# Optimization experiments

Hardware: AMD Instinct MI355X
Metric: run time of the kernel (lower is better)

Reference implementation:

```python
import jax, jax.numpy as jnp
import numpy as np

B, C, H, W = 4, 256, 160, 160
N = 512
REID = 128
NUM_LAYERS = 2
BINS = 7          # adaptive_avg_pool2d target (7,7)
EPS_BN = 1e-5
EPS_NORM = 1e-12  # torch F.normalize eps


def setup_inputs() -> dict:
    key = jax.random.key(0)
    ks = jax.random.split(key, 8)
    x = jax.random.normal(ks[0], (B, C, H, W), jnp.float32)
    # valid normalized boxes: x1,y1 in [0,0.7], w,h in [0.1,0.3]
    xy1 = jax.random.uniform(ks[1], (B, N, 2), minval=0.0, maxval=0.7)
    wh = jax.random.uniform(ks[2], (B, N, 2), minval=0.1, maxval=0.3)
    bboxes = jnp.concatenate([xy1, jnp.minimum(xy1 + wh, 1.0)], axis=-1)
    # conv stack params (kaiming-ish init), BN in eval mode with running stats
    conv_w = jax.random.normal(ks[3], (NUM_LAYERS, C, C, 3, 3), jnp.float32) * np.sqrt(2.0 / (C * 9)).astype(np.float32)
    conv_b = jnp.zeros((NUM_LAYERS, C), jnp.float32)
    bn_gamma = jnp.ones((NUM_LAYERS, C), jnp.float32)
    bn_beta = jnp.zeros((NUM_LAYERS, C), jnp.float32)
    bn_mean = jnp.zeros((NUM_LAYERS, C), jnp.float32)
    bn_var = jnp.ones((NUM_LAYERS, C), jnp.float32)
    # reid_embedding MLP: Linear(C, C//2) -> ReLU -> Dropout(eval) -> Linear(C//2, REID)
    w1 = jax.random.normal(ks[4], (C // 2, C), jnp.float32) * 0.01
    b1 = jnp.zeros((C // 2,), jnp.float32)
    w2 = jax.random.normal(ks[5], (REID, C // 2), jnp.float32) * 0.01
    b2 = jnp.zeros((REID,), jnp.float32)
    return dict(x=x, bboxes=bboxes, conv_w=conv_w, conv_b=conv_b,
                bn_gamma=bn_gamma, bn_beta=bn_beta, bn_mean=bn_mean, bn_var=bn_var,
                w1=w1, b1=b1, w2=w2, b2=b2)


def _conv_bn_relu(x, w, b, gamma, beta, mean, var):
    y = jax.lax.conv_general_dilated(
        x, w, window_strides=(1, 1), padding=((1, 1), (1, 1)),
        dimension_numbers=('NCHW', 'OIHW', 'NCHW')) + b[None, :, None, None]
    scale = (gamma / jnp.sqrt(var + EPS_BN))[None, :, None, None]
    y = (y - mean[None, :, None, None]) * scale + beta[None, :, None, None]
    return jax.nn.relu(y)


def _roi_pool(S, box):
    # S: (C, H+1, W+1) integral image of the feature map; box: (4,) = x1,y1,x2,y2 in [0,1]
    x1 = jnp.clip(jnp.floor(box[0] * W).astype(jnp.int32), 0, W)
    y1 = jnp.clip(jnp.floor(box[1] * H).astype(jnp.int32), 0, H)
    x2 = jnp.clip(jnp.floor(box[2] * W).astype(jnp.int32), 0, W)
    y2 = jnp.clip(jnp.floor(box[3] * H).astype(jnp.int32), 0, H)
    valid = (x2 > x1) & (y2 > y1)
    hl = jnp.maximum(y2 - y1, 1)
    wl = jnp.maximum(x2 - x1, 1)
    i = jnp.arange(BINS)
    # PyTorch adaptive_avg_pool2d binning: [floor(i*L/B), ceil((i+1)*L/B))
    hs = y1 + (i * hl) // BINS
    he = y1 + ((i + 1) * hl + BINS - 1) // BINS
    ws = x1 + (i * wl) // BINS
    we = x1 + ((i + 1) * wl + BINS - 1) // BINS
    # bin sums via integral image -> (C, 7, 7)
    s = (S[:, he[:, None], we[None, :]] - S[:, hs[:, None], we[None, :]]
         - S[:, he[:, None], ws[None, :]] + S[:, hs[:, None], ws[None, :]])
    area = ((he - hs)[:, None] * (we - ws)[None, :]).astype(S.dtype)
    # adaptive 7x7 avg pool, then global avg pool over the 7x7 grid
    pooled = jnp.mean(s / area, axis=(1, 2))  # (C,)
    return pooled, valid


def reference(x, bboxes, conv_w, conv_b, bn_gamma, bn_beta, bn_mean, bn_var, w1, b1, w2, b2):
    f = x
    for l in range(NUM_LAYERS):
        f = _conv_bn_relu(f, conv_w[l], conv_b[l], bn_gamma[l], bn_beta[l], bn_mean[l], bn_var[l])
    # integral image, zero-padded: S[b,c,y,x] = sum of f[b,c,:y,:x] -> (B, C, H+1, W+1)
    S = jnp.pad(jnp.cumsum(jnp.cumsum(f, axis=2), axis=3), ((0, 0), (0, 0), (1, 0), (1, 0)))
    pooled, valid = jax.vmap(jax.vmap(_roi_pool, in_axes=(None, 0)), in_axes=(0, 0))(S, bboxes)
    # reid_embedding MLP (dropout is identity in eval)
    h = jax.nn.relu(jnp.einsum('bnc,hc->bnh', pooled, w1) + b1)
    feat = jnp.einsum('bnh,rh->bnr', h, w2) + b2
    feat = jnp.where(valid[..., None], feat, jnp.zeros((), feat.dtype))
    norm = jnp.maximum(jnp.linalg.norm(feat, axis=-1, keepdims=True), EPS_NORM)
    return feat / norm
```

## Files before the change

### kernel.cpp

```cpp
#include <hip/hip_runtime.h>
#include <hip/hip_bf16.h>

typedef __attribute__((ext_vector_type(8))) short s16x8;
typedef __attribute__((ext_vector_type(4))) float f32x4;


__device__ __forceinline__ void async_ld16(const void* g, void* l) {
  __builtin_amdgcn_global_load_lds(
      (const __attribute__((address_space(1))) void*)g,
      (__attribute__((address_space(3))) void*)l, 16, 0, 0);
}

__global__ __launch_bounds__(256) void prep_all(
    const float* __restrict__ x,
    __hip_bfloat16* __restrict__ xpad, __hip_bfloat16* __restrict__ f1,
    const float* __restrict__ cw, __hip_bfloat16* __restrict__ wpk,
    const float* __restrict__ cb, const float* __restrict__ g,
    const float* __restrict__ bt, const float* __restrict__ mn,
    const float* __restrict__ vr, float* __restrict__ ab,
    const float* __restrict__ w1, const float* __restrict__ w2,
    float* __restrict__ w1t, float* __restrict__ w2t) {
  __shared__ float tile[32][33];
  int bi = blockIdx.x;
  if (bi < 12800) {
    int blk = bi;
    int xt = blk % 5;
    int ct = (blk / 5) & 7;
    int by = blk / 40;
    int b = by / 80, yp = by - (by / 80) * 80;
    int tx = threadIdx.x & 31, ty = threadIdx.x >> 5;
#pragma unroll
    for (int ry = 0; ry < 2; ++ry) {
      int y = yp * 2 + ry;
      const float* src = x + (((size_t)(b * 256 + ct * 32)) * 160 + y) * 160 + xt * 32 + tx;
#pragma unroll
      for (int k = 0; k < 4; k++) tile[ty * 4 + k][tx] = src[(size_t)(ty * 4 + k) * 25600];
      __syncthreads();
      __hip_bfloat16* dst =
          xpad + (((size_t)(b * 162 + y + 1)) * 162 + (xt * 32 + 1)) * 256 + ct * 32 + tx;
#pragma unroll
      for (int k = 0; k < 4; k++) {
        int xx = ty * 4 + k;
        dst[(size_t)xx * 256] = __float2bfloat16(tile[tx][xx]);
      }
      __syncthreads();
    }
  } else if (bi < 17952) {
    int e0 = bi - 12800;
    int buf = e0 / 2576; int rem = e0 - buf * 2576;
    int b = rem / 644;   int e = rem - b * 644;
    int y, xx;
    if (e < 162)      { y = 0;           xx = e; }
    else if (e < 324) { y = 161;         xx = e - 162; }
    else if (e < 484) { y = e - 324 + 1; xx = 0; }
    else              { y = e - 484 + 1; xx = 161; }
    __hip_bfloat16* p = (buf ? f1 : xpad) + (((size_t)b * 162 + y) * 162 + xx) * 256 + threadIdx.x;
    *p = __float2bfloat16(0.f);
  } else if (bi < 22560) {
    int t = (bi - 17952) * 256 + threadIdx.x;
    int ci = t & 255, co = (t >> 8) & 255, rest = t >> 16;
    int tap = rest % 9, lyr = rest / 9;
    int dy = tap / 3, dx = tap - dy * 3;
    float v = cw[((((size_t)lyr * 256 + co) * 256 + ci) * 3 + dy) * 3 + dx];
    wpk[(((size_t)lyr * 9 + tap) * 256 + co) * 256 + ci] = __float2bfloat16(v);
  } else if (bi < 22562) {
    int t = (bi - 22560) * 256 + threadIdx.x;
    float a = g[t] / sqrtf(vr[t] + 1e-5f);
    ab[t] = a;
    ab[512 + t] = (cb[t] - mn[t]) * a + bt[t];
  } else {
    int t = (bi - 22562) * 256 + threadIdx.x;
    if (t < 32768) {
      int h = t >> 8, k = t & 255;
      w1t[k * 128 + h] = w1[h * 256 + k];
    } else {
      int u = t - 32768;
      int r = u >> 7, k = u & 127;
      w2t[k * 128 + r] = w2[r * 128 + k];
    }
  }
}

__global__ __launch_bounds__(256, 2) void conv_bn_relu(
    const __hip_bfloat16* __restrict__ inp, __hip_bfloat16* __restrict__ outp,
    const __hip_bfloat16* __restrict__ wpk,
    const float* __restrict__ alpha, const float* __restrict__ beff) {
  __shared__ __align__(16) short As[128 * 64];
  __shared__ __align__(16) short Bs[256 * 64];
  const int t = threadIdx.x;
  const int mtile = ((blockIdx.x & 7) * 100) + (blockIdx.x >> 3);
  const int l = t & 63;
  const int wv = t >> 6;
  const int lr = l & 15, lq = l >> 4;
  const int wm = wv >> 1, wn = wv & 1;

  const int srow = t >> 3;
  const int koff = (((t & 7) ^ (srow & 7)) << 3);
  const short* inS = (const short*)inp;
  const short* wS = (const short*)wpk;
  long abase[4];
#pragma unroll
  for (int i = 0; i < 4; i++) {
    int p = mtile * 128 + i * 32 + srow;
    int b = p / 25600; int r = p - b * 25600; int y = r / 160; int x = r - y * 160;
    abase[i] = (((long)b * 162 + y) * 162 + x) * 256 + koff;
  }
  const long bbase = ((long)srow) * 256 + koff;

  f32x4 acc[4][8];
#pragma unroll
  for (int i = 0; i < 4; i++)
#pragma unroll
    for (int j = 0; j < 8; j++) acc[i][j] = (f32x4){0.f, 0.f, 0.f, 0.f};

#pragma unroll 1
  for (int u = 0; u < 36; ++u) {
    const int tap = u >> 2, kc = u & 3;
    const int dy = tap / 3, dx = tap - dy * 3;
    const long aoff = ((long)(dy * 162 + dx)) * 256 + kc * 64;
    const long boff = (long)tap * 65536 + kc * 64;
    __syncthreads();
#pragma unroll
    for (int i = 0; i < 4; i++)
      async_ld16(inS + abase[i] + aoff, As + i * 2048 + t * 8);
#pragma unroll
    for (int j = 0; j < 8; j++)
      async_ld16(wS + bbase + boff + (long)j * 8192, Bs + j * 2048 + t * 8);
    __syncthreads();
#pragma unroll
    for (int kk = 0; kk < 2; ++kk) {
      const int ps = (((kk << 2) | lq) ^ (lr & 7)) << 3;
      s16x8 av[4], bv[8];
#pragma unroll
      for (int mi = 0; mi < 4; ++mi)
        av[mi] = *(const s16x8*)&As[(wm * 64 + mi * 16 + lr) * 64 + ps];
#pragma unroll
      for (int ni = 0; ni < 8; ++ni)
        bv[ni] = *(const s16x8*)&Bs[(wn * 128 + ni * 16 + lr) * 64 + ps];
#pragma unroll
      for (int mi = 0; mi < 4; ++mi)
#pragma unroll
        for (int ni = 0; ni < 8; ++ni)
          acc[mi][ni] = __builtin_amdgcn_mfma_f32_16x16x32_bf16(av[mi], bv[ni], acc[mi][ni], 0, 0, 0);
    }
  }

  float al[8], be_[8];
#pragma unroll
  for (int ni = 0; ni < 8; ++ni) {
    int co = wn * 128 + ni * 16 + lr;
    al[ni] = alpha[co];
    be_[ni] = beff[co];
  }
#pragma unroll
  for (int mi = 0; mi < 4; ++mi) {
    int prow = mtile * 128 + wm * 64 + mi * 16 + lq * 4;
#pragma unroll
    for (int j = 0; j < 4; ++j) {
      int p = prow + j;
      int b = p / 25600; int r = p - b * 25600; int y = r / 160; int x = r - y * 160;
      long ob = (((long)b * 162 + (y + 1)) * 162 + (x + 1)) * 256 + wn * 128;
#pragma unroll
      for (int ni = 0; ni < 8; ++ni) {
        float v = acc[mi][ni][j] * al[ni] + be_[ni];
        outp[ob + ni * 16 + lr] = __float2bfloat16(fmaxf(v, 0.f));
      }
    }
  }
}

__global__ __launch_bounds__(128) void cumsum_w(const __hip_bfloat16* __restrict__ f2,
                                                float* __restrict__ S) {
  int row = blockIdx.x;
  int b = row / 160, y = row - (row / 160) * 160;
  int cp = threadIdx.x;
  const unsigned* src =
      (const unsigned*)((const short*)f2 + (((size_t)b * 162 + y + 1) * 162 + 1) * 256) + cp;
  float2* dst = (float2*)(S + (((size_t)b * 161 + y + 1) * 161) * 256) + cp;
  dst[0] = float2{0.f, 0.f};
  float r0 = 0.f, r1 = 0.f;
  for (int x8 = 0; x8 < 160; x8 += 8) {
    unsigned v[8];
#pragma unroll
    for (int k = 0; k < 8; k++) v[k] = src[(size_t)(x8 + k) * 128];
#pragma unroll
    for (int k = 0; k < 8; k++) {
      r0 += __uint_as_float((v[k] & 0xffffu) << 16);
      r1 += __uint_as_float(v[k] & 0xffff0000u);
      dst[(size_t)(x8 + k + 1) * 128] = float2{r0, r1};
    }
  }
}

__global__ __launch_bounds__(256) void cumsum_h(float* __restrict__ S) {
  int bi = blockIdx.x;
  int b = bi / 161, q = bi - (bi / 161) * 161;
  int c = threadIdx.x;
  float* col = S + (((size_t)b * 161) * 161 + q) * 256 + c;
  const size_t ys = (size_t)161 * 256;
  col[0] = 0.f;
  float run = 0.f;
  for (int y0 = 1; y0 <= 160; y0 += 16) {
    float v[16];
#pragma unroll
    for (int k = 0; k < 16; k++) v[k] = col[(size_t)(y0 + k) * ys];
#pragma unroll
    for (int k = 0; k < 16; k++) { run += v[k]; col[(size_t)(y0 + k) * ys] = run; }
  }
}

__global__ __launch_bounds__(256) void roi_mlp(const float* __restrict__ S,
                                               const float* __restrict__ bbox,
                                               const float* __restrict__ w1t,
                                               const float* __restrict__ b1,
                                               const float* __restrict__ w2t,
                                               const float* __restrict__ b2,
                                               float* __restrict__ out) {
  int bn = blockIdx.x;
  int b = bn >> 9;
  int t = threadIdx.x;
  __shared__ float pl[256];
  __shared__ float hh[128];
  __shared__ float red[2];

  float bx1 = bbox[bn * 4 + 0], by1 = bbox[bn * 4 + 1];
  float bx2 = bbox[bn * 4 + 2], by2 = bbox[bn * 4 + 3];
  int x1 = min(max((int)floorf(bx1 * 160.f), 0), 160);
  int y1 = min(max((int)floorf(by1 * 160.f), 0), 160);
  int x2 = min(max((int)floorf(bx2 * 160.f), 0), 160);
  int y2 = min(max((int)floorf(by2 * 160.f), 0), 160);
  int vld = (x2 > x1 && y2 > y1) ? 1 : 0;
  int hl = max(y2 - y1, 1), wl = max(x2 - x1, 1);
  int hs[7], he[7], ws_[7], we_[7];
  float rh[7], rw[7];
#pragma unroll
  for (int i = 0; i < 7; i++) {
    hs[i] = y1 + (i * hl) / 7;
    he[i] = y1 + ((i + 1) * hl + 6) / 7;
    rh[i] = 1.f / (float)(he[i] - hs[i]);
    ws_[i] = x1 + (i * wl) / 7;
    we_[i] = x1 + ((i + 1) * wl + 6) / 7;
    rw[i] = 1.f / (float)(we_[i] - ws_[i]);
  }
  const float* Sb = S + (size_t)b * 161 * 161 * 256 + t;
  float acc = 0.f;
#pragma unroll
  for (int i = 0; i < 7; i++) {
    const float* rE = Sb + (size_t)he[i] * (161 * 256);
    const float* rS = Sb + (size_t)hs[i] * (161 * 256);
#pragma unroll
    for (int j = 0; j < 7; j++) {
      size_t qe = (size_t)we_[j] * 256, qs = (size_t)ws_[j] * 256;
      float s = rE[qe] - rS[qe] - rE[qs] + rS[qs];
      acc += s * (rh[i] * rw[j]);
    }
  }
  pl[t] = acc * (1.f / 49.f);
  __syncthreads();

  float a = 0.f;
  if (t < 128) {
    a = b1[t];
#pragma unroll 8
    for (int k = 0; k < 256; k++) a += w1t[k * 128 + t] * pl[k];
    hh[t] = fmaxf(a, 0.f);
  }
  __syncthreads();
  float f = 0.f;
  if (t < 128) {
    f = b2[t];
#pragma unroll 8
    for (int k = 0; k < 128; k++) f += w2t[k * 128 + t] * hh[k];
    if (!vld) f = 0.f;
    float ss = f * f;
#pragma unroll
    for (int off = 32; off > 0; off >>= 1) ss += __shfl_xor(ss, off);
    if ((t & 63) == 0) red[t >> 6] = ss;
  }
  __syncthreads();
  if (t < 128) {
    float nrm = fmaxf(sqrtf(red[0] + red[1]), 1e-12f);
    out[(size_t)bn * 128 + t] = f / nrm;
  }
}

extern "C" void kernel_launch(void* const* d_in, const int* in_sizes, int n_in,
                              void* d_out, int out_size, void* d_ws, size_t ws_size,
                              hipStream_t stream) {
  const float* x = (const float*)d_in[0];
  const float* bboxes = (const float*)d_in[1];
  const float* conv_w = (const float*)d_in[2];
  const float* conv_b = (const float*)d_in[3];
  const float* bn_g = (const float*)d_in[4];
  const float* bn_b = (const float*)d_in[5];
  const float* bn_m = (const float*)d_in[6];
  const float* bn_v = (const float*)d_in[7];
  const float* w1 = (const float*)d_in[8];
  const float* b1 = (const float*)d_in[9];
  const float* w2 = (const float*)d_in[10];
  const float* b2 = (const float*)d_in[11];

  char* ws = (char*)d_ws;
  const size_t PADB = (size_t)4 * 162 * 162 * 256 * 2;
  const size_t WPKB = (size_t)2 * 9 * 256 * 256 * 2;
  const size_t SB = (size_t)4 * 161 * 161 * 256 * 4;

  __hip_bfloat16* xpad = (__hip_bfloat16*)(ws);
  __hip_bfloat16* f1 = (__hip_bfloat16*)(ws + PADB);
  __hip_bfloat16* wpk = (__hip_bfloat16*)(ws + 2 * PADB);
  float* abuf = (float*)(ws + 2 * PADB + WPKB);
  float* S = (float*)(ws + 2 * PADB + WPKB + 4096);
  float* w1t = (float*)(ws + 2 * PADB + WPKB + 4096 + SB);
  float* w2t = w1t + 32768;

  prep_all<<<22754, 256, 0, stream>>>(x, xpad, f1, conv_w, wpk, conv_b, bn_g, bn_b, bn_m,
                                      bn_v, abuf, w1, w2, w1t, w2t);

  conv_bn_relu<<<800, 256, 0, stream>>>(xpad, f1, wpk, abuf, abuf + 512);
  conv_bn_relu<<<800, 256, 0, stream>>>(f1, xpad, wpk + (size_t)9 * 256 * 256, abuf + 256, abuf + 768);

  cumsum_w<<<640, 128, 0, stream>>>(xpad, S);
  cumsum_h<<<644, 256, 0, stream>>>(S);
  roi_mlp<<<2048, 256, 0, stream>>>(S, bboxes, w1t, b1, w2t, b2, (float*)d_out);
}
```

Before: 396.4 us.

## Vectorize input transpose-pack and process two ROIs per block in roi_mlp

The NCHW-to-padded-NHWC bf16 conversion now reads float4 rows for two channels at once, packs channel pairs into 32-bit words in shared memory, and writes 32-bit words, using one row per block instead of two with fewer syncs. roi_mlp now handles two boxes per 256-thread block, each half looping over channels twice, so all threads stay busy in the MLP stages and half as many blocks are launched. Both changes aim to cut memory-transaction count and idle lanes in kernels outside the conv. They add more integral-image gathers per thread in the pooling stage.

```diff
diff --git a/kernel.cpp b/kernel.cpp
--- a/kernel.cpp
+++ b/kernel.cpp
@@ -20,30 +20,34 @@
     const float* __restrict__ vr, float* __restrict__ ab,
     const float* __restrict__ w1, const float* __restrict__ w2,
     float* __restrict__ w1t, float* __restrict__ w2t) {
-  __shared__ float tile[32][33];
+  __shared__ unsigned tile_u[32][33];
   int bi = blockIdx.x;
+  int t = threadIdx.x;
   if (bi < 12800) {
-    int blk = bi;
-    int xt = blk % 5;
-    int ct = (blk / 5) & 7;
-    int by = blk / 40;
-    int b = by / 80, yp = by - (by / 80) * 80;
-    int tx = threadIdx.x & 31, ty = threadIdx.x >> 5;
-#pragma unroll
-    for (int ry = 0; ry < 2; ++ry) {
-      int y = yp * 2 + ry;
-      const float* src = x + (((size_t)(b * 256 + ct * 32)) * 160 + y) * 160 + xt * 32 + tx;
-#pragma unroll
-      for (int k = 0; k < 4; k++) tile[ty * 4 + k][tx] = src[(size_t)(ty * 4 + k) * 25600];
-      __syncthreads();
-      __hip_bfloat16* dst =
-          xpad + (((size_t)(b * 162 + y + 1)) * 162 + (xt * 32 + 1)) * 256 + ct * 32 + tx;
-#pragma unroll
-      for (int k = 0; k < 4; k++) {
-        int xx = ty * 4 + k;
-        dst[(size_t)xx * 256] = __float2bfloat16(tile[tx][xx]);
-      }
-      __syncthreads();
+    int xt = bi % 5;
+    int cq = (bi / 5) & 3;
+    int by = bi / 20;
+    int b = by / 160, y = by - (by / 160) * 160;
+    int p = t >> 3, q = t & 7;
+    int c0 = cq * 64 + 2 * p;
+    const float* row = x + (((size_t)(b * 256 + c0)) * 160 + y) * 160 + xt * 32 + q * 4;
+    float4 v0 = *(const float4*)row;
+    float4 v1 = *(const float4*)(row + 25600);
+#pragma unroll
+    for (int k = 0; k < 4; k++) {
+      float vk0 = (&v0.x)[k], vk1 = (&v1.x)[k];
+      __hip_bfloat16 lo = __float2bfloat16(vk0), hi = __float2bfloat16(vk1);
+      tile_u[p][q * 4 + k] =
+          (unsigned)*(unsigned short*)&lo | ((unsigned)*(unsigned short*)&hi << 16);
+    }
+    __syncthreads();
+    int s = t & 31, xh = t >> 5;
+    unsigned* dstu = (unsigned*)xpad;
+#pragma unroll
+    for (int xr = 0; xr < 4; xr++) {
+      int xx = xr * 8 + xh;
+      size_t du = (((size_t)(b * 162 + y + 1)) * 162 + 1 + xt * 32 + xx) * 128 + cq * 32 + s;
+      dstu[du] = tile_u[s][xx];
     }
   } else if (bi < 17952) {
     int e0 = bi - 12800;
@@ -54,27 +58,27 @@
     else if (e < 324) { y = 161;         xx = e - 162; }
     else if (e < 484) { y = e - 324 + 1; xx = 0; }
     else              { y = e - 484 + 1; xx = 161; }
-    __hip_bfloat16* p = (buf ? f1 : xpad) + (((size_t)b * 162 + y) * 162 + xx) * 256 + threadIdx.x;
+    __hip_bfloat16* p = (buf ? f1 : xpad) + (((size_t)b * 162 + y) * 162 + xx) * 256 + t;
     *p = __float2bfloat16(0.f);
   } else if (bi < 22560) {
-    int t = (bi - 17952) * 256 + threadIdx.x;
-    int ci = t & 255, co = (t >> 8) & 255, rest = t >> 16;
+    int tt = (bi - 17952) * 256 + t;
+    int ci = tt & 255, co = (tt >> 8) & 255, rest = tt >> 16;
     int tap = rest % 9, lyr = rest / 9;
     int dy = tap / 3, dx = tap - dy * 3;
     float v = cw[((((size_t)lyr * 256 + co) * 256 + ci) * 3 + dy) * 3 + dx];
     wpk[(((size_t)lyr * 9 + tap) * 256 + co) * 256 + ci] = __float2bfloat16(v);
   } else if (bi < 22562) {
-    int t = (bi - 22560) * 256 + threadIdx.x;
-    float a = g[t] / sqrtf(vr[t] + 1e-5f);
-    ab[t] = a;
-    ab[512 + t] = (cb[t] - mn[t]) * a + bt[t];
+    int tt = (bi - 22560) * 256 + t;
+    float a = g[tt] / sqrtf(vr[tt] + 1e-5f);
+    ab[tt] = a;
+    ab[512 + tt] = (cb[tt] - mn[tt]) * a + bt[tt];
   } else {
-    int t = (bi - 22562) * 256 + threadIdx.x;
-    if (t < 32768) {
-      int h = t >> 8, k = t & 255;
+    int tt = (bi - 22562) * 256 + t;
+    if (tt < 32768) {
+      int h = tt >> 8, k = tt & 255;
       w1t[k * 128 + h] = w1[h * 256 + k];
     } else {
-      int u = t - 32768;
+      int u = tt - 32768;
       int r = u >> 7, k = u & 127;
       w2t[k * 128 + r] = w2[r * 128 + k];
     }
@@ -216,12 +220,13 @@
                                                const float* __restrict__ w2t,
                                                const float* __restrict__ b2,
                                                float* __restrict__ out) {
-  int bn = blockIdx.x;
+  int t = threadIdx.x;
+  int box = t >> 7;
+  int bn = blockIdx.x * 2 + box;
   int b = bn >> 9;
-  int t = threadIdx.x;
-  __shared__ float pl[256];
-  __shared__ float hh[128];
-  __shared__ float red[2];
+  __shared__ float pl[2][256];
+  __shared__ float hh[2][128];
+  __shared__ float red[2][2];
 
   float bx1 = bbox[bn * 4 + 0], by1 = bbox[bn * 4 + 1];
   float bx2 = bbox[bn * 4 + 2], by2 = bbox[bn * 4 + 3];
@@ -242,46 +247,44 @@
     we_[i] = x1 + ((i + 1) * wl + 6) / 7;
     rw[i] = 1.f / (float)(we_[i] - ws_[i]);
   }
-  const float* Sb = S + (size_t)b * 161 * 161 * 256 + t;
-  float acc = 0.f;
-#pragma unroll
-  for (int i = 0; i < 7; i++) {
-    const float* rE = Sb + (size_t)he[i] * (161 * 256);
-    const float* rS = Sb + (size_t)hs[i] * (161 * 256);
-#pragma unroll
-    for (int j = 0; j < 7; j++) {
-      size_t qe = (size_t)we_[j] * 256, qs = (size_t)ws_[j] * 256;
-      float s = rE[qe] - rS[qe] - rE[qs] + rS[qs];
-      acc += s * (rh[i] * rw[j]);
-    }
-  }
-  pl[t] = acc * (1.f / 49.f);
+#pragma unroll
+  for (int iter = 0; iter < 2; iter++) {
+    int c = (t & 127) + iter * 128;
+    const float* Sb = S + (size_t)b * 161 * 161 * 256 + c;
+    float acc = 0.f;
+#pragma unroll
+    for (int i = 0; i < 7; i++) {
+      const float* rE = Sb + (size_t)he[i] * (161 * 256);
+      const float* rS = Sb + (size_t)hs[i] * (161 * 256);
+#pragma unroll
+      for (int j = 0; j < 7; j++) {
+        size_t qe = (size_t)we_[j] * 256, qs = (size_t)ws_[j] * 256;
+        float s = rE[qe] - rS[qe] - rE[qs] + rS[qs];
+        acc += s * (rh[i] * rw[j]);
+      }
+    }
+    pl[box][c] = acc * (1.f / 49.f);
+  }
   __syncthreads();
 
-  float a = 0.f;
-  if (t < 128) {
-    a = b1[t];
+  int unit = t & 127;
+  float a = b1[unit];
 #pragma unroll 8
-    for (int k = 0; k < 256; k++) a += w1t[k * 128 + t] * pl[k];
-    hh[t] = fmaxf(a, 0.f);
-  }
+  for (int k = 0; k < 256; k++) a += w1t[k * 128 + unit] * pl[box][k];
+  hh[box][unit] = fmaxf(a, 0.f);
   __syncthreads();
-  float f = 0.f;
-  if (t < 128) {
-    f = b2[t];
+
+  float f = b2[unit];
 #pragma unroll 8
-    for (int k = 0; k < 128; k++) f += w2t[k * 128 + t] * hh[k];
-    if (!vld) f = 0.f;
-    float ss = f * f;
-#pragma unroll
-    for (int off = 32; off > 0; off >>= 1) ss += __shfl_xor(ss, off);
-    if ((t & 63) == 0) red[t >> 6] = ss;
-  }
+  for (int k = 0; k < 128; k++) f += w2t[k * 128 + unit] * hh[box][k];
+  if (!vld) f = 0.f;
+  float ss = f * f;
+#pragma unroll
+  for (int off = 32; off > 0; off >>= 1) ss += __shfl_xor(ss, off);
+  if ((t & 63) == 0) red[box][(t >> 6) & 1] = ss;
   __syncthreads();
-  if (t < 128) {
-    float nrm = fmaxf(sqrtf(red[0] + red[1]), 1e-12f);
-    out[(size_t)bn * 128 + t] = f / nrm;
-  }
+  float nrm = fmaxf(sqrtf(red[box][0] + red[box][1]), 1e-12f);
+  out[(size_t)bn * 128 + unit] = f / nrm;
 }
 
 extern "C" void kernel_launch(void* const* d_in, const int* in_sizes, int n_in,
@@ -321,5 +324,5 @@
 
   cumsum_w<<<640, 128, 0, stream>>>(xpad, S);
   cumsum_h<<<644, 256, 0, stream>>>(S);
-  roi_mlp<<<2048, 256, 0, stream>>>(S, bboxes, w1t, b1, w2t, b2, (float*)d_out);
-}
+  roi_mlp<<<1024, 256, 0, stream>>>(S, bboxes, w1t, b1, w2t, b2, (float*)d_out);
+}
```

Measured after the change: 437.7 us. +10.4%, slower.
